# Optimization experiments

Hardware: AMD Instinct MI355X
Metric: run time of the kernel (lower is better)

## Reference

```python
import jax, jax.numpy as jnp
import numpy as np

B, C, H, W = 16, 128, 128, 128


def _gram(feat):
    # feat: [B, C, H, W] -> [B, C, HW]; gram: [B, C, C]
    f = feat.reshape(feat.shape[0], feat.shape[1], -1)
    return jnp.einsum('bcn,bdn->bcd', f, f)


def setup_inputs() -> dict:
    key = jax.random.key(0)
    k1, k2 = jax.random.split(key)
    feat = jax.random.normal(k1, (B, C, H, W), dtype=jnp.float32)
    feat_decod = jax.random.normal(k2, (B, C, H, W), dtype=jnp.float32)
    return {"feat": feat, "feat_decod": feat_decod}


def reference(feat, feat_decod):
    feat_size = feat.shape[2] * feat.shape[3]  # H*W
    feat_nb = feat.shape[1]                     # C
    gram_enc = _gram(feat)
    gram_dec = _gram(feat_decod)
    diff = gram_dec - gram_enc
    # per-sample scalar loss: [B]
    denom = 4.0 * feat_size * feat_size * feat_nb * feat_nb
    return jnp.sum(diff * diff, axis=(-2, -1)) / denom
```

## Files before the change

kernel.cpp:

```cpp
#include <hip/hip_runtime.h>
#include <hip/hip_bf16.h>


typedef __attribute__((ext_vector_type(8))) short short8;
typedef __attribute__((ext_vector_type(4))) float f32x4;

#define CC 128
#define NN 16384

__device__ __forceinline__ short f2bf(float x) {
    unsigned u = __builtin_bit_cast(unsigned, x);
    u += 0x7fffu + ((u >> 16) & 1u);
    return (short)(u >> 16);
}

__global__ __launch_bounds__(256, 2) void gram_partial_k(
    const float* __restrict__ f0, const float* __restrict__ f1,
    float* __restrict__ partials, int S, int Kc, int nst)
{
    __shared__ short lds[2][CC * 128];

    const int tid = threadIdx.x;
    const int bx  = blockIdx.x;
    const int g   = bx & 31;
    const int s   = bx >> 5;

    const float* src  = (g & 1) ? f1 : f0;
    const float* base = src + (size_t)(g >> 1) * ((size_t)CC * NN) + (size_t)s * Kc;

    const int srow = tid >> 4;
    const int scb  = tid & 15;
    const float* gp = base + (size_t)srow * NN + scb * 8;

    const int lane = tid & 63;
    const int w    = tid >> 6;
    const int m0   = (w & 1) * 64;
    const int n0   = (w >> 1) * 64;
    const int lr   = lane & 15;
    const int lk   = lane >> 4;

    const int rot = bx & (nst - 1);

    f32x4 acc[4][4];
    #pragma unroll
    for (int i = 0; i < 4; ++i)
        #pragma unroll
        for (int j = 0; j < 4; ++j)
            acc[i][j] = (f32x4){0.f, 0.f, 0.f, 0.f};

    float4 ra[8], rb[8];

    auto load_stage = [&](int st) {
        int sp = (st + rot) & (nst - 1);
        #pragma unroll
        for (int it = 0; it < 8; ++it) {
            const float* p = gp + (size_t)it * 16 * NN + (size_t)sp * 128;
            ra[it] = *(const float4*)p;
            rb[it] = *(const float4*)(p + 4);
        }
    };

    auto store_stage = [&](int buf) {
        #pragma unroll
        for (int it = 0; it < 8; ++it) {
            int r = srow + 16 * it;
            short8 v = { f2bf(ra[it].x), f2bf(ra[it].y), f2bf(ra[it].z), f2bf(ra[it].w),
                         f2bf(rb[it].x), f2bf(rb[it].y), f2bf(rb[it].z), f2bf(rb[it].w) };
            int phys = scb ^ (r & 15);
            *(short8*)&lds[buf][r * 128 + phys * 8] = v;
        }
    };

    auto compute = [&](int buf) {
        #pragma unroll
        for (int ks = 0; ks < 4; ++ks) {
            short8 af[4], bfr[4];
            int cb = ks * 4 + lk;
            #pragma unroll
            for (int i = 0; i < 4; ++i) {
                int r = m0 + i * 16 + lr;
                af[i] = *(const short8*)&lds[buf][r * 128 + ((cb ^ (r & 15)) * 8)];
            }
            #pragma unroll
            for (int i = 0; i < 4; ++i) {
                int r = n0 + i * 16 + lr;
                bfr[i] = *(const short8*)&lds[buf][r * 128 + ((cb ^ (r & 15)) * 8)];
            }
            #pragma unroll
            for (int mi = 0; mi < 4; ++mi)
                #pragma unroll
                for (int ni = 0; ni < 4; ++ni)
                    acc[mi][ni] = __builtin_amdgcn_mfma_f32_16x16x32_bf16(
                        af[mi], bfr[ni], acc[mi][ni], 0, 0, 0);
        }
    };

    load_stage(0);
    store_stage(0);
    __syncthreads();
    for (int st = 0; st < nst; ++st) {
        int cur = st & 1;
        bool more = (st + 1 < nst);
        if (more) load_stage(st + 1);
        compute(cur);
        if (more) store_stage(cur ^ 1);
        __syncthreads();
    }

    float* op = partials + ((size_t)g * S + s) * (CC * CC);
    #pragma unroll
    for (int mi = 0; mi < 4; ++mi)
        #pragma unroll
        for (int ni = 0; ni < 4; ++ni)
            #pragma unroll
            for (int i = 0; i < 4; ++i) {
                int row = m0 + mi * 16 + lk * 4 + i;
                int col = n0 + ni * 16 + lr;
                op[row * CC + col] = acc[mi][ni][i];
            }
}

__global__ __launch_bounds__(256) void reduce1_k(
    const float* __restrict__ partials, float* __restrict__ part2, int S)
{
    int b     = blockIdx.x >> 4;
    int chunk = blockIdx.x & 15;
    int t     = threadIdx.x;
    size_t e  = (size_t)chunk * 1024 + (size_t)t * 4;

    const f32x4* Pe = (const f32x4*)(partials + ((size_t)(2 * b) * S) * (CC * CC) + e);
    const f32x4* Pd = (const f32x4*)(partials + ((size_t)(2 * b + 1) * S) * (CC * CC) + e);
    const size_t stride = (size_t)CC * CC / 4;

    f32x4 ae = {0.f, 0.f, 0.f, 0.f}, ad = {0.f, 0.f, 0.f, 0.f};
    if (S == 16) {
        #pragma unroll
        for (int s2 = 0; s2 < 16; ++s2) {
            ae += Pe[(size_t)s2 * stride];
            ad += Pd[(size_t)s2 * stride];
        }
    } else {
        for (int s2 = 0; s2 < S; ++s2) {
            ae += Pe[(size_t)s2 * stride];
            ad += Pd[(size_t)s2 * stride];
        }
    }
    f32x4 d = ad - ae;
    float v = d[0] * d[0] + d[1] * d[1] + d[2] * d[2] + d[3] * d[3];
    #pragma unroll
    for (int off = 32; off > 0; off >>= 1) v += __shfl_down(v, off);
    __shared__ float wsum[4];
    if ((t & 63) == 0) wsum[t >> 6] = v;
    __syncthreads();
    if (t == 0) part2[b * 16 + chunk] = wsum[0] + wsum[1] + wsum[2] + wsum[3];
}

__global__ void reduce2_k(const float* __restrict__ part2, float* __restrict__ out)
{
    int b = blockIdx.x;
    int t = threadIdx.x;
    float v = (t < 16) ? part2[b * 16 + t] : 0.f;
    #pragma unroll
    for (int off = 8; off > 0; off >>= 1) v += __shfl_down(v, off);
    if (t == 0) out[b] = v * (1.0f / 17592186044416.0f);
}

extern "C" void kernel_launch(void* const* d_in, const int* in_sizes, int n_in,
                              void* d_out, int out_size, void* d_ws, size_t ws_size,
                              hipStream_t stream)
{
    const float* f0 = (const float*)d_in[0];
    const float* f1 = (const float*)d_in[1];
    float* out = (float*)d_out;

    const size_t perS = 32ull * CC * CC * 4;
    const size_t tail = 16 * 16 * 4;
    int S = 16;
    while (S > 1 && perS * (size_t)S + tail > ws_size) S >>= 1;
    int Kc  = NN / S;
    int nst = Kc / 128;

    float* partials = (float*)d_ws;
    float* part2    = (float*)((char*)d_ws + perS * (size_t)S);

    gram_partial_k<<<32 * S, 256, 0, stream>>>(f0, f1, partials, S, Kc, nst);
    reduce1_k<<<16 * 16, 256, 0, stream>>>(partials, part2, S);
    reduce2_k<<<16, 64, 0, stream>>>(part2, out);
}
```

Baseline: 289.7 us.

## Use async global-to-LDS loads with 4-stage pipeline and 512-thread blocks

Replaces the register-staged load, bf16 convert and LDS store with direct global_load_lds transfers of fp32 tiles into a 4-buffer LDS ring. Each K step shrinks to 32, and loads run three stages ahead, with vmcnt waits and raw barriers. Blocks grow to 8 waves, each owning a 64x32 output tile, and the bf16 conversion moves to after the LDS read. The aim is to hide global memory latency and cut register pressure so more waves fit. The cost is repeated conversions (A tiles are converted by each wave sharing them), fp32 LDS traffic twice as large, and a barrier every 32 elements of K.

```diff
diff --git a/kernel.cpp b/kernel.cpp
--- a/kernel.cpp
+++ b/kernel.cpp
@@ -14,11 +14,14 @@
     return (short)(u >> 16);
 }
 
-__global__ __launch_bounds__(256, 2) void gram_partial_k(
+#define WAITV(N) asm volatile("s_waitcnt vmcnt(" #N ")" ::: "memory")
+#define BAR() do { __builtin_amdgcn_s_barrier(); __builtin_amdgcn_sched_barrier(0); } while (0)
+
+__global__ __launch_bounds__(512, 4) void gram_partial_k(
     const float* __restrict__ f0, const float* __restrict__ f1,
     float* __restrict__ partials, int S, int Kc, int nst)
 {
-    __shared__ short lds[2][CC * 128];
+    __shared__ float lds_f[4 * 128 * 32];
 
     const int tid = threadIdx.x;
     const int bx  = blockIdx.x;
@@ -28,90 +31,94 @@
     const float* src  = (g & 1) ? f1 : f0;
     const float* base = src + (size_t)(g >> 1) * ((size_t)CC * NN) + (size_t)s * Kc;
 
-    const int srow = tid >> 4;
-    const int scb  = tid & 15;
-    const float* gp = base + (size_t)srow * NN + scb * 8;
-
     const int lane = tid & 63;
     const int w    = tid >> 6;
     const int m0   = (w & 1) * 64;
-    const int n0   = (w >> 1) * 64;
+    const int n0   = ((w >> 1) & 3) * 32;
     const int lr   = lane & 15;
     const int lk   = lane >> 4;
 
-    const int rot = bx & (nst - 1);
+    const int r0  = 0 * 64 + w * 8 + (lane >> 3);
+    const int r1  = 1 * 64 + w * 8 + (lane >> 3);
+    const int cb0 = (lane & 7) ^ (r0 & 7);
+    const int cb1 = (lane & 7) ^ (r1 & 7);
+    const float* gb0 = base + (size_t)r0 * NN + cb0 * 4;
+    const float* gb1 = base + (size_t)r1 * NN + cb1 * 4;
 
-    f32x4 acc[4][4];
+    auto issue_stage = [&](int st) {
+        int buf = st & 3;
+        const float* g0 = gb0 + (size_t)st * 32;
+        const float* g1 = gb1 + (size_t)st * 32;
+        __builtin_amdgcn_global_load_lds(
+            (const __attribute__((address_space(1))) void*)g0,
+            (__attribute__((address_space(3))) void*)&lds_f[buf * 4096 + 0 * 2048 + w * 256],
+            16, 0, 0);
+        __builtin_amdgcn_global_load_lds(
+            (const __attribute__((address_space(1))) void*)g1,
+            (__attribute__((address_space(3))) void*)&lds_f[buf * 4096 + 1 * 2048 + w * 256],
+            16, 0, 0);
+    };
+
+    f32x4 acc[4][2];
     #pragma unroll
     for (int i = 0; i < 4; ++i)
         #pragma unroll
-        for (int j = 0; j < 4; ++j)
+        for (int j = 0; j < 2; ++j)
             acc[i][j] = (f32x4){0.f, 0.f, 0.f, 0.f};
 
-    float4 ra[8], rb[8];
-
-    auto load_stage = [&](int st) {
-        int sp = (st + rot) & (nst - 1);
+    auto compute = [&](int st) {
+        int buf = st & 3;
+        const float* lb = &lds_f[buf * 4096];
+        short8 af[4], bf2[2];
         #pragma unroll
-        for (int it = 0; it < 8; ++it) {
-            const float* p = gp + (size_t)it * 16 * NN + (size_t)sp * 128;
-            ra[it] = *(const float4*)p;
-            rb[it] = *(const float4*)(p + 4);
+        for (int i = 0; i < 4; ++i) {
+            int row = m0 + i * 16 + lr;
+            int c0  = (lk * 2)     ^ (row & 7);
+            int c1  = (lk * 2 + 1) ^ (row & 7);
+            float4 x0 = *(const float4*)&lb[row * 32 + c0 * 4];
+            float4 x1 = *(const float4*)&lb[row * 32 + c1 * 4];
+            af[i] = (short8){ f2bf(x0.x), f2bf(x0.y), f2bf(x0.z), f2bf(x0.w),
+                              f2bf(x1.x), f2bf(x1.y), f2bf(x1.z), f2bf(x1.w) };
         }
+        #pragma unroll
+        for (int j2 = 0; j2 < 2; ++j2) {
+            int row = n0 + j2 * 16 + lr;
+            int c0  = (lk * 2)     ^ (row & 7);
+            int c1  = (lk * 2 + 1) ^ (row & 7);
+            float4 x0 = *(const float4*)&lb[row * 32 + c0 * 4];
+            float4 x1 = *(const float4*)&lb[row * 32 + c1 * 4];
+            bf2[j2] = (short8){ f2bf(x0.x), f2bf(x0.y), f2bf(x0.z), f2bf(x0.w),
+                                f2bf(x1.x), f2bf(x1.y), f2bf(x1.z), f2bf(x1.w) };
+        }
+        #pragma unroll
+        for (int mi = 0; mi < 4; ++mi)
+            #pragma unroll
+            for (int ni = 0; ni < 2; ++ni)
+                acc[mi][ni] = __builtin_amdgcn_mfma_f32_16x16x32_bf16(
+                    af[mi], bf2[ni], acc[mi][ni], 0, 0, 0);
     };
 
-    auto store_stage = [&](int buf) {
-        #pragma unroll
-        for (int it = 0; it < 8; ++it) {
-            int r = srow + 16 * it;
-            short8 v = { f2bf(ra[it].x), f2bf(ra[it].y), f2bf(ra[it].z), f2bf(ra[it].w),
-                         f2bf(rb[it].x), f2bf(rb[it].y), f2bf(rb[it].z), f2bf(rb[it].w) };
-            int phys = scb ^ (r & 15);
-            *(short8*)&lds[buf][r * 128 + phys * 8] = v;
-        }
-    };
+    issue_stage(0);
+    issue_stage(1);
+    issue_stage(2);
+    WAITV(4);
+    BAR();
 
-    auto compute = [&](int buf) {
-        #pragma unroll
-        for (int ks = 0; ks < 4; ++ks) {
-            short8 af[4], bfr[4];
-            int cb = ks * 4 + lk;
-            #pragma unroll
-            for (int i = 0; i < 4; ++i) {
-                int r = m0 + i * 16 + lr;
-                af[i] = *(const short8*)&lds[buf][r * 128 + ((cb ^ (r & 15)) * 8)];
-            }
-            #pragma unroll
-            for (int i = 0; i < 4; ++i) {
-                int r = n0 + i * 16 + lr;
-                bfr[i] = *(const short8*)&lds[buf][r * 128 + ((cb ^ (r & 15)) * 8)];
-            }
-            #pragma unroll
-            for (int mi = 0; mi < 4; ++mi)
-                #pragma unroll
-                for (int ni = 0; ni < 4; ++ni)
-                    acc[mi][ni] = __builtin_amdgcn_mfma_f32_16x16x32_bf16(
-                        af[mi], bfr[ni], acc[mi][ni], 0, 0, 0);
-        }
-    };
-
-    load_stage(0);
-    store_stage(0);
-    __syncthreads();
-    for (int st = 0; st < nst; ++st) {
-        int cur = st & 1;
-        bool more = (st + 1 < nst);
-        if (more) load_stage(st + 1);
-        compute(cur);
-        if (more) store_stage(cur ^ 1);
-        __syncthreads();
+    for (int j = 0; j < nst - 3; ++j) {
+        issue_stage(j + 3);
+        compute(j);
+        WAITV(4);
+        BAR();
     }
+    compute(nst - 3); WAITV(2); BAR();
+    compute(nst - 2); WAITV(0); BAR();
+    compute(nst - 1);
 
     float* op = partials + ((size_t)g * S + s) * (CC * CC);
     #pragma unroll
     for (int mi = 0; mi < 4; ++mi)
         #pragma unroll
-        for (int ni = 0; ni < 4; ++ni)
+        for (int ni = 0; ni < 2; ++ni)
             #pragma unroll
             for (int i = 0; i < 4; ++i) {
                 int row = m0 + mi * 16 + lk * 4 + i;
@@ -178,12 +185,12 @@
     int S = 16;
     while (S > 1 && perS * (size_t)S + tail > ws_size) S >>= 1;
     int Kc  = NN / S;
-    int nst = Kc / 128;
+    int nst = Kc / 32;
 
     float* partials = (float*)d_ws;
     float* part2    = (float*)((char*)d_ws + perS * (size_t)S);
 
-    gram_partial_k<<<32 * S, 256, 0, stream>>>(f0, f1, partials, S, Kc, nst);
+    gram_partial_k<<<32 * S, 512, 0, stream>>>(f0, f1, partials, S, Kc, nst);
     reduce1_k<<<16 * 16, 256, 0, stream>>>(partials, part2, S);
     reduce2_k<<<16, 64, 0, stream>>>(part2, out);
 }
```

Result: slower. 316.9 us (+9.4%).
